# Performance work log

Hardware: AMD Instinct MI355X
Metric: run time of the kernel (lower is better)

Reference implementation:

```python
import jax, jax.numpy as jnp
import numpy as np

EPS = 1e-5
K = 3

def _bn(x, g, b):
    # training-mode BatchNorm2d: batch stats over (N,H,W), biased variance
    m = jnp.mean(x, axis=(0, 2, 3), keepdims=True)
    v = jnp.var(x, axis=(0, 2, 3), keepdims=True)
    return (x - m) * jax.lax.rsqrt(v + EPS) * g[None, :, None, None] + b[None, :, None, None]

def _gelu(x):
    return jax.nn.gelu(x, approximate=False)

def _dyn_dw(x, aw1, ab1, aw2, ab2):
    # dynamic depthwise conv: per-sample k^2 softmax weights shared over channels
    b, c, h, w = x.shape
    gap = jnp.mean(x, axis=(2, 3))                              # (b,c)
    h1 = jax.nn.relu(jnp.einsum('oc,bc->bo', aw1, gap) + ab1)   # (b,c//8)
    kw = jax.nn.softmax(jnp.einsum('oc,bc->bo', aw2, h1) + ab2, axis=1)  # (b,k^2)
    xp = jnp.pad(x, ((0, 0), (0, 0), (1, 1), (1, 1)))
    out = jnp.zeros_like(x)
    idx = 0
    for i in range(K):
        for j in range(K):
            out = out + kw[:, idx, None, None, None] * xp[:, :, i:i + h, j:j + w]
            idx += 1
    return out

def _channel_att(x, w1, w2):
    avg = jnp.mean(x, axis=(2, 3))        # (b,C)
    mx = jnp.max(x, axis=(2, 3))          # (b,C)
    def fc(v):
        return jnp.einsum('oc,bc->bo', w2, jax.nn.relu(jnp.einsum('oc,bc->bo', w1, v)))
    s = jax.nn.sigmoid(fc(avg) + fc(mx))  # (b,C)
    return s[:, :, None, None] * x

def _forward(x, w1, b1, g1, be1, aw1, ab1, aw2, ab2, g2, be2,
             ca_w1, ca_w2, pw, pb, g3, be3, sw, sb):
    b, n, d = x.shape
    h = w = int(np.sqrt(n))
    residual = x
    xi = jnp.transpose(x.reshape(b, h, w, d), (0, 3, 1, 2))       # (b,d,h,w)
    # pw_expand: 1x1 conv -> GELU -> BN
    y = jnp.einsum('oc,bchw->bohw', w1, xi) + b1[None, :, None, None]
    y = _bn(_gelu(y), g1, be1)                                    # (b,4d,h,w)
    # dw_conv: dynamic depthwise -> GELU -> BN -> channel attention
    y = _dyn_dw(y, aw1, ab1, aw2, ab2)
    y = _bn(_gelu(y), g2, be2)
    y = _channel_att(y, ca_w1, ca_w2)
    # spatial attention
    avg_o = jnp.mean(y, axis=1, keepdims=True)
    max_o = jnp.max(y, axis=1, keepdims=True)
    sp_in = jnp.concatenate([avg_o, max_o], axis=1)               # (b,2,h,w)
    sp = jax.lax.conv_general_dilated(sp_in, sw, (1, 1), ((3, 3), (3, 3)),
                                      dimension_numbers=('NCHW', 'OIHW', 'NCHW'))
    sp = jax.nn.sigmoid(sp + sb[None, :, None, None])
    y = y * sp
    # pw_project: 1x1 conv -> BN
    y = jnp.einsum('oc,bchw->bohw', pw, y) + pb[None, :, None, None]
    y = _bn(y, g3, be3)
    y = jnp.transpose(y, (0, 2, 3, 1)).reshape(b, n, d)
    return residual + y

def setup_inputs() -> dict:
    key = jax.random.key(0)
    ks = jax.random.split(key, 16)
    d, C = 256, 1024
    def rn(k, shape, fan):
        return jax.random.normal(k, shape, jnp.float32) * np.float32(np.sqrt(2.0 / fan))
    return {
        'x': jax.random.normal(ks[0], (8, 1024, d), jnp.float32),
        'w1': rn(ks[1], (C, d), d), 'b1': jnp.zeros((C,), jnp.float32),
        'g1': jnp.ones((C,), jnp.float32), 'be1': jnp.zeros((C,), jnp.float32),
        'aw1': rn(ks[2], (C // 8, C), C), 'ab1': jnp.zeros((C // 8,), jnp.float32),
        'aw2': rn(ks[3], (K * K, C // 8), C // 8), 'ab2': jnp.zeros((K * K,), jnp.float32),
        'g2': jnp.ones((C,), jnp.float32), 'be2': jnp.zeros((C,), jnp.float32),
        'ca_w1': rn(ks[4], (C // 16, C), C), 'ca_w2': rn(ks[5], (C, C // 16), C // 16),
        'pw': rn(ks[6], (d, C), C), 'pb': jnp.zeros((d,), jnp.float32),
        'g3': jnp.ones((d,), jnp.float32), 'be3': jnp.zeros((d,), jnp.float32),
        'sw': rn(ks[7], (1, 2, 7, 7), 2 * 49), 'sb': jnp.zeros((1,), jnp.float32),
    }

def reference(x, w1, b1, g1, be1, aw1, ab1, aw2, ab2, g2, be2,
              ca_w1, ca_w2, pw, pb, g3, be3, sw, sb):
    return _forward(x, w1, b1, g1, be1, aw1, ab1, aw2, ab2, g2, be2,
                    ca_w1, ca_w2, pw, pb, g3, be3, sw, sb)
```

## Files before the change

### kernel.cpp

```cpp
#include <hip/hip_runtime.h>
#include <math.h>

constexpr int B = 8;
constexpr int D = 256;
constexpr int C = 1024;
constexpr int H = 32, W = 32;
constexpr int P = H * W;
constexpr int M = B * P;
constexpr float EPS = 1e-5f;

typedef unsigned short u16;
typedef unsigned int u32;
typedef __attribute__((ext_vector_type(8))) short short8;
typedef __attribute__((ext_vector_type(4))) float floatx4;

constexpr size_t WS_CHSUM1 = 0;
constexpr size_t WS_CHSQ1  = 1024;
constexpr size_t WS_GAPSUM = 2048;
constexpr size_t WS_CHSUM3 = 10240;
constexpr size_t WS_CHSQ3  = 10496;
constexpr size_t WS_CHSUM2 = 10752;
constexpr size_t WS_CHSQ2  = 11776;
constexpr size_t WS_BSUM2  = 12800;
constexpr size_t WS_UMAX2  = 20992;
constexpr size_t WS_UMAXN2 = 29184;
constexpr size_t WS_ACC_COUNT = 37376;
constexpr size_t WS_SCALE1 = 37376;
constexpr size_t WS_SHIFT1 = 38400;
constexpr size_t WS_KW     = 39424;
constexpr size_t WS_SCALE2 = 39680;
constexpr size_t WS_SHIFT2 = 40704;
constexpr size_t WS_SATT   = 41728;
constexpr size_t WS_AVGO   = 49920;
constexpr size_t WS_MAXO   = 58112;
constexpr size_t WS_SP     = 66304;
constexpr size_t WS_PRE    = 74496;
constexpr size_t WS_T1B    = 2171648;
constexpr size_t WS_T2B    = 6365952;
constexpr size_t WS_XB     = 10560256;
constexpr size_t WS_W1B    = 11608832;
constexpr size_t WS_PWB    = 11739904;
constexpr size_t WS_PWBF   = 11870976;
constexpr size_t WS_BIAS2  = 12919552;

__device__ __forceinline__ float gelu_exact(float v) {
    return 0.5f * v * (1.0f + erff(v * 0.70710678118654752440f));
}

__device__ __forceinline__ u16 f2bf(float f) {
    u32 u = __float_as_uint(f);
    u += 0x7fff + ((u >> 16) & 1);
    return (u16)(u >> 16);
}

__device__ __forceinline__ float bf2f(u16 v) {
    return __uint_as_float(((u32)v) << 16);
}

__device__ __forceinline__ u32 fkey(float f) {
    u32 u = __float_as_uint(f);
    return (u & 0x80000000u) ? ~u : (u | 0x80000000u);
}
__device__ __forceinline__ float fkeyinv(u32 k) {
    return __uint_as_float((k & 0x80000000u) ? (k ^ 0x80000000u) : ~k);
}

#define GLOAD(SRC, DST) __builtin_amdgcn_global_load_lds( \
    (const __attribute__((address_space(1))) void*)(SRC), \
    (__attribute__((address_space(3))) void*)(DST), 16, 0, 0)

__global__ __launch_bounds__(256) void cvt_all_kernel(const float* __restrict__ x,
                                                      const float* __restrict__ w1,
                                                      u16* __restrict__ xb,
                                                      u16* __restrict__ w1b,
                                                      float* __restrict__ acc_zero) {
    const int i = blockIdx.x * 256 + threadIdx.x;
    if (i < (int)WS_ACC_COUNT) acc_zero[i] = 0.f;
    const float* src;
    u16* dst;
    int off;
    if (i < 524288) { src = x;  dst = xb;  off = i; }
    else            { src = w1; dst = w1b; off = i - 524288; }
    const float4 v = *(const float4*)(src + (size_t)off * 4);
    uint2 o;
    o.x = ((u32)f2bf(v.x)) | ((u32)f2bf(v.y) << 16);
    o.y = ((u32)f2bf(v.z)) | ((u32)f2bf(v.w) << 16);
    *(uint2*)(dst + (size_t)off * 4) = o;
}

template<int KD, int EPI, int NS, int MB, int NB>
__global__ __launch_bounds__(256) void mfma_gemm_kernel(
    const u16* __restrict__ A,
    const u16* __restrict__ Bw,
    const float* __restrict__ bias,
    const float* __restrict__ rowscale,
    void* __restrict__ outv,
    float* __restrict__ csum,
    float* __restrict__ csq,
    float* __restrict__ gsum)
{
    constexpr int MI = MB / 32;
    constexpr int NJ = NB / 32;
    constexpr int ABUF = MB * 32;
    constexpr int BBUF = NB * 32;
    constexpr int BUFSZ = ABUF + BBUF;
    constexpr int GA = MB / 64;
    constexpr int GB = NB / 64;
    constexpr int LD = GA + GB;
    constexpr int NCH = KD / 32;
    constexpr int GX = NS / NB;
    constexpr int NWG = (M / MB) * GX;
    constexpr int CPX = NWG / 8;
    extern __shared__ u16 smem[];
    const int t = threadIdx.x;
    const int lane = t & 63;

    const int lin = blockIdx.y * GX + blockIdx.x;
    const int swz = (lin & 7) * CPX + (lin >> 3);
    const int bx = swz % GX;
    const int by = swz / GX;
    const int row0 = by * MB;
    const int col0 = bx * NB;
    const int bb = row0 >> 10;

    const int wv = t >> 6;
    const int wrow = (wv >> 1) * (MB / 2);
    const int wcol = (wv & 1) * (NB / 2);
    const int lm = lane & 15;
    const int lk8 = (lane >> 4) * 8;
    const int srow = t >> 2;
    const int scol = (t & 3) * 8;
    const u16* gA = A + (size_t)(row0 + srow) * KD + scol;
    const u16* gB = Bw + (EPI == 1 ? (size_t)bb * NS * KD : (size_t)0)
                       + (size_t)(col0 + srow) * KD + scol;
    const float* biasp = bias + (EPI == 1 ? bb * NS : 0);

    const floatx4 zero = {0.f, 0.f, 0.f, 0.f};
    floatx4 acc[MI][NJ];
#pragma unroll
    for (int i = 0; i < MI; ++i)
#pragma unroll
        for (int j = 0; j < NJ; ++j) acc[i][j] = zero;

    auto stage = [&](u16* buf, int c) {
        const int kk = c * 32;
        u16* As = buf;
        u16* Bs = buf + ABUF;
#pragma unroll
        for (int g = 0; g < GA; ++g)
            GLOAD(gA + (size_t)g * 64 * KD + kk, As + g * 2048 + t * 8);
#pragma unroll
        for (int g = 0; g < GB; ++g)
            GLOAD(gB + (size_t)g * 64 * KD + kk, Bs + g * 2048 + t * 8);
    };
    auto compute = [&](const u16* buf) {
        const u16* As = buf;
        const u16* Bs = buf + ABUF;
        short8 af[MI], bf[NJ];
#pragma unroll
        for (int i = 0; i < MI; ++i)
            af[i] = *(const short8*)(As + (wrow + i * 16 + lm) * 32 + lk8);
#pragma unroll
        for (int j = 0; j < NJ; ++j)
            bf[j] = *(const short8*)(Bs + (wcol + j * 16 + lm) * 32 + lk8);
#pragma unroll
        for (int i = 0; i < MI; ++i)
#pragma unroll
            for (int j = 0; j < NJ; ++j)
                acc[i][j] = __builtin_amdgcn_mfma_f32_16x16x32_bf16(af[i], bf[j], acc[i][j], 0, 0, 0);
    };

    stage(smem, 0);
    for (int c = 0; c < NCH; ++c) {
        u16* curb = smem + (c & 1) * BUFSZ;
        if (c + 1 < NCH) {
            stage(smem + ((c + 1) & 1) * BUFSZ, c + 1);
            if constexpr (LD == 2) asm volatile("s_waitcnt vmcnt(2)" ::: "memory");
            else                   asm volatile("s_waitcnt vmcnt(3)" ::: "memory");
        } else {
            asm volatile("s_waitcnt vmcnt(0)" ::: "memory");
        }
        __builtin_amdgcn_s_barrier();
        compute(curb);
        asm volatile("s_waitcnt lgkmcnt(0)" ::: "memory");
        __builtin_amdgcn_s_barrier();
    }

    float colsum[NJ], colsq[NJ];
#pragma unroll
    for (int j = 0; j < NJ; ++j) { colsum[j] = 0.f; colsq[j] = 0.f; }

    if (EPI == 0) {
        u16* Cs = smem;
#pragma unroll
        for (int i = 0; i < MI; ++i) {
#pragma unroll
            for (int r = 0; r < 4; ++r) {
                const int lrow = wrow + i * 16 + (lane >> 4) * 4 + r;
#pragma unroll
                for (int j = 0; j < NJ; ++j) {
                    const int lcol = wcol + j * 16 + lm;
                    const float tv = gelu_exact(acc[i][j][r] + biasp[col0 + lcol]);
                    Cs[lrow * NB + lcol] = f2bf(tv);
                    colsum[j] += tv;
                    colsq[j] = fmaf(tv, tv, colsq[j]);
                }
            }
        }
        __syncthreads();
        constexpr int TPR = NB / 8;
        constexpr int RPP = 256 / TPR;
        u16* outp = (u16*)outv;
#pragma unroll
        for (int pp = 0; pp < MB / RPP; ++pp) {
            const int r = pp * RPP + t / TPR;
            const int cc = (t % TPR) * 8;
            *(uint4*)(outp + (size_t)(row0 + r) * NS + col0 + cc) =
                *(const uint4*)(Cs + r * NB + cc);
        }
    } else {
        float* Cs = (float*)smem;
#pragma unroll
        for (int i = 0; i < MI; ++i) {
#pragma unroll
            for (int r = 0; r < 4; ++r) {
                const int lrow = wrow + i * 16 + (lane >> 4) * 4 + r;
                const float rs = rowscale[row0 + lrow];
#pragma unroll
                for (int j = 0; j < NJ; ++j) {
                    const int lcol = wcol + j * 16 + lm;
                    const float tv = rs * (acc[i][j][r] + biasp[col0 + lcol]);
                    Cs[lrow * NB + lcol] = tv;
                    colsum[j] += tv;
                    colsq[j] = fmaf(tv, tv, colsq[j]);
                }
            }
        }
        __syncthreads();
        constexpr int TPR = NB / 4;
        constexpr int RPP = 256 / TPR;
        float* outp = (float*)outv;
#pragma unroll
        for (int pp = 0; pp < MB / RPP; ++pp) {
            const int r = pp * RPP + t / TPR;
            const int cc = (t % TPR) * 4;
            *(float4*)(outp + (size_t)(row0 + r) * NS + col0 + cc) =
                *(const float4*)(Cs + r * NB + cc);
        }
    }

#pragma unroll
    for (int j = 0; j < NJ; ++j) {
        float s = colsum[j];
        float q = colsq[j];
        s += __shfl_xor(s, 16); s += __shfl_xor(s, 32);
        q += __shfl_xor(q, 16); q += __shfl_xor(q, 32);
        if (lane < 16) {
            const int c = col0 + wcol + j * 16 + lm;
            atomicAdd(&csum[c], s);
            atomicAdd(&csq[c], q);
            if (EPI == 0) atomicAdd(&gsum[bb * NS + c], s);
        }
    }
}

__global__ __launch_bounds__(1024) void dynmlp_kernel(const float* __restrict__ chsum1,
                                                      const float* __restrict__ chsq1,
                                                      const float* __restrict__ gapsum,
                                                      const float* __restrict__ g1,
                                                      const float* __restrict__ be1,
                                                      const float* __restrict__ aw1,
                                                      const float* __restrict__ ab1,
                                                      const float* __restrict__ aw2,
                                                      const float* __restrict__ ab2,
                                                      float* __restrict__ scale1,
                                                      float* __restrict__ shift1,
                                                      float* __restrict__ kw) {
    const int b = blockIdx.x;
    const int t = threadIdx.x;
    const int wave = t >> 6, lane = t & 63;
    __shared__ float g[1024];
    __shared__ float h1[128];
    __shared__ float logits[12];
    {
        const float m = chsum1[t] * (1.0f / (float)M);
        const float var = chsq1[t] * (1.0f / (float)M) - m * m;
        const float rstd = rsqrtf(var + EPS);
        const float sc = rstd * g1[t];
        const float sh = be1[t] - m * sc;
        if (b == 0) { scale1[t] = sc; shift1[t] = sh; }
        g[t] = gapsum[b * C + t] * (1.0f / (float)P) * sc + sh;
    }
    __syncthreads();
#pragma unroll
    for (int k = 0; k < 8; ++k) {
        const int u = wave * 8 + k;
        const float4* wr = (const float4*)(aw1 + (size_t)u * C);
        float s = 0.f;
#pragma unroll
        for (int ch = 0; ch < 4; ++ch) {
            const float4 wv = wr[lane + 64 * ch];
            const float4 sv = *(const float4*)(g + 4 * lane + 256 * ch);
            s += wv.x * sv.x + wv.y * sv.y + wv.z * sv.z + wv.w * sv.w;
        }
#pragma unroll
        for (int off = 1; off < 64; off <<= 1) s += __shfl_xor(s, off);
        if (lane == 0) h1[u] = fmaxf(s + ab1[u], 0.f);
    }
    __syncthreads();
    if (wave < 9) {
        float s = aw2[wave * 128 + lane] * h1[lane]
                + aw2[wave * 128 + 64 + lane] * h1[64 + lane];
#pragma unroll
        for (int off = 1; off < 64; off <<= 1) s += __shfl_xor(s, off);
        if (lane == 0) logits[wave] = s + ab2[wave];
    }
    __syncthreads();
    if (t == 0) {
        float mx = logits[0];
        for (int i = 1; i < 9; ++i) mx = fmaxf(mx, logits[i]);
        float e[9], den = 0.f;
        for (int i = 0; i < 9; ++i) { e[i] = expf(logits[i] - mx); den += e[i]; }
        const float inv = 1.0f / den;
        for (int i = 0; i < 9; ++i) kw[b * 9 + i] = e[i] * inv;
    }
}

__global__ __launch_bounds__(256) void dwconv_kernel(const u16* __restrict__ t1b,
                                                     const float* __restrict__ scale1,
                                                     const float* __restrict__ shift1,
                                                     const float* __restrict__ kw,
                                                     u16* __restrict__ t2b,
                                                     float* __restrict__ chsum2,
                                                     float* __restrict__ chsq2,
                                                     float* __restrict__ bsum2,
                                                     u32* __restrict__ umax2,
                                                     u32* __restrict__ umaxn2) {
    __shared__ u16 rows[3 * 32 * 256];
    const int lin = blockIdx.y * 4 + blockIdx.x;
    const int swz = (lin & 7) * 128 + (lin >> 3);
    const int cq = swz & 3;
    const int bh = swz >> 2;
    const int b = bh >> 5;
    const int h = bh & 31;
    const int t = threadIdx.x;

    const u16* gbase = t1b + (size_t)b * P * C + cq * 256;
#pragma unroll
    for (int i = 0; i < 12; ++i) {
        const int lin2 = i * 256 + t;
        const int chunk = lin2 >> 5;
        const int r = chunk >> 5;
        const int w = chunk & 31;
        const int off8 = (lin2 & 31) * 8;
        const int hr = h + r - 1;
        uint4 v = {0u, 0u, 0u, 0u};
        if (hr >= 0 && hr < H)
            v = *(const uint4*)(gbase + (size_t)(hr * W + w) * C + off8);
        *(uint4*)(&rows[chunk * 256 + off8]) = v;
    }
    __syncthreads();

    const int c = t;
    const int gc = cq * 256 + c;
    float kk[9];
#pragma unroll
    for (int i = 0; i < 9; ++i) kk[i] = kw[b * 9 + i];
    const float sc = scale1[gc];
    const float sh = shift1[gc];
    float scm[3], shm[3];
    scm[0] = (h > 0)     ? sc : 0.f;  shm[0] = (h > 0)     ? sh : 0.f;
    scm[1] = sc;                      shm[1] = sh;
    scm[2] = (h < H - 1) ? sc : 0.f;  shm[2] = (h < H - 1) ? sh : 0.f;

    const u16* rp0 = rows + c;
#define DWVAL(ri, w) fmaf(bf2f(rp0[((ri) * 32 + (w)) * 256]), scm[ri], shm[ri])

    float vm0 = 0.f, vm1 = 0.f, vm2 = 0.f;
    float vc0 = DWVAL(0, 0), vc1 = DWVAL(1, 0), vc2 = DWVAL(2, 0);
    float vp0 = DWVAL(0, 1), vp1 = DWVAL(1, 1), vp2 = DWVAL(2, 1);

    float s = 0.f, q = 0.f, mx = -INFINITY, mn = INFINITY;
    u16* orow = t2b + ((size_t)b * P + h * W) * C + gc;
    for (int w = 0; w < W; ++w) {
        float acc;
        acc = kk[0] * vm0;
        acc = fmaf(kk[1], vc0, acc);
        acc = fmaf(kk[2], vp0, acc);
        acc = fmaf(kk[3], vm1, acc);
        acc = fmaf(kk[4], vc1, acc);
        acc = fmaf(kk[5], vp1, acc);
        acc = fmaf(kk[6], vm2, acc);
        acc = fmaf(kk[7], vc2, acc);
        acc = fmaf(kk[8], vp2, acc);
        const float y = gelu_exact(acc);
        orow[(size_t)w * C] = f2bf(y);
        s += y;
        q = fmaf(y, y, q);
        mx = fmaxf(mx, y);
        mn = fminf(mn, y);
        vm0 = vc0; vc0 = vp0;
        vm1 = vc1; vc1 = vp1;
        vm2 = vc2; vc2 = vp2;
        if (w + 2 < W) {
            vp0 = DWVAL(0, w + 2);
            vp1 = DWVAL(1, w + 2);
            vp2 = DWVAL(2, w + 2);
        } else {
            vp0 = 0.f; vp1 = 0.f; vp2 = 0.f;
        }
    }
#undef DWVAL
    atomicAdd(&chsum2[gc], s);
    atomicAdd(&chsq2[gc], q);
    atomicAdd(&bsum2[b * C + gc], s);
    atomicMax(&umax2[b * C + gc], fkey(mx));
    atomicMax(&umaxn2[b * C + gc], fkey(-mn));
}

__global__ __launch_bounds__(1024) void chatt_kernel(const float* __restrict__ chsum2,
                                                     const float* __restrict__ chsq2,
                                                     const float* __restrict__ bsum2,
                                                     const u32* __restrict__ umax2,
                                                     const u32* __restrict__ umaxn2,
                                                     const float* __restrict__ g2,
                                                     const float* __restrict__ be2,
                                                     const float* __restrict__ caw1,
                                                     const float* __restrict__ caw2,
                                                     float* __restrict__ scale2,
                                                     float* __restrict__ shift2,
                                                     float* __restrict__ s_att) {
    const int b = blockIdx.x;
    const int t = threadIdx.x;
    const int wave = t >> 6, lane = t & 63;
    __shared__ float la[1024], lx[1024], ha[64], hm[64];
    {
        const float m = chsum2[t] * (1.0f / (float)M);
        const float var = chsq2[t] * (1.0f / (float)M) - m * m;
        const float rstd = rsqrtf(var + EPS);
        const float sc = rstd * g2[t];
        const float sh = be2[t] - m * sc;
        if (b == 0) { scale2[t] = sc; shift2[t] = sh; }
        la[t] = bsum2[b * C + t] * (1.0f / (float)P) * sc + sh;
        const float mx = fkeyinv(umax2[b * C + t]);
        const float mn = -fkeyinv(umaxn2[b * C + t]);
        lx[t] = (sc >= 0.f ? mx : mn) * sc + sh;
    }
    __syncthreads();
#pragma unroll
    for (int k = 0; k < 8; ++k) {
        const int u = wave * 8 + k;
        const int row = u & 63;
        const float* src = (u < 64) ? la : lx;
        const float4* wr = (const float4*)(caw1 + (size_t)row * C);
        float s = 0.f;
#pragma unroll
        for (int ch = 0; ch < 4; ++ch) {
            const float4 wv = wr[lane + 64 * ch];
            const float4 sv = *(const float4*)(src + 4 * lane + 256 * ch);
            s += wv.x * sv.x + wv.y * sv.y + wv.z * sv.z + wv.w * sv.w;
        }
#pragma unroll
        for (int off = 1; off < 64; off <<= 1) s += __shfl_xor(s, off);
        if (lane == 0) {
            s = fmaxf(s, 0.f);
            if (u < 64) ha[row] = s; else hm[row] = s;
        }
    }
    __syncthreads();
    {
        const float4* w2 = (const float4*)(caw2 + (size_t)t * 64);
        float s = 0.f;
#pragma unroll
        for (int j = 0; j < 16; ++j) {
            const float4 wv = w2[j];
            s += wv.x * (ha[j * 4 + 0] + hm[j * 4 + 0]);
            s += wv.y * (ha[j * 4 + 1] + hm[j * 4 + 1]);
            s += wv.z * (ha[j * 4 + 2] + hm[j * 4 + 2]);
            s += wv.w * (ha[j * 4 + 3] + hm[j * 4 + 3]);
        }
        s_att[b * C + t] = 1.0f / (1.0f + expf(-s));
    }
}

__global__ __launch_bounds__(256) void fold_kernel(const float* __restrict__ pw,
                                                   const float* __restrict__ pb,
                                                   const float* __restrict__ scale2,
                                                   const float* __restrict__ shift2,
                                                   const float* __restrict__ s_att,
                                                   u16* __restrict__ pwb,
                                                   float* __restrict__ bias2) {
    const int bd = blockIdx.x;
    const int b = bd >> 8;
    const int d = bd & 255;
    const int t = threadIdx.x;
    const int c0 = t * 4;
    const float4 wv = *(const float4*)(pw + (size_t)d * C + c0);
    const float4 sc = *(const float4*)(scale2 + c0);
    const float4 sh = *(const float4*)(shift2 + c0);
    const float4 sa = *(const float4*)(s_att + (size_t)b * C + c0);
    uint2 o;
    o.x = ((u32)f2bf(wv.x * sc.x * sa.x)) | ((u32)f2bf(wv.y * sc.y * sa.y) << 16);
    o.y = ((u32)f2bf(wv.z * sc.z * sa.z)) | ((u32)f2bf(wv.w * sc.w * sa.w) << 16);
    *(uint2*)(pwb + ((size_t)b * D + d) * C + c0) = o;
    float s = wv.x * sh.x * sa.x + wv.y * sh.y * sa.y
            + wv.z * sh.z * sa.z + wv.w * sh.w * sa.w;
#pragma unroll
    for (int off = 1; off < 64; off <<= 1) s += __shfl_xor(s, off);
    __shared__ float ps[4];
    const int wave = t >> 6, lane = t & 63;
    if (lane == 0) ps[wave] = s;
    __syncthreads();
    if (t == 0) bias2[bd] = pb[d] + ps[0] + ps[1] + ps[2] + ps[3];
}

__global__ __launch_bounds__(256) void yq_kernel(const u16* __restrict__ t2b,
                                                 const float* __restrict__ scale2,
                                                 const float* __restrict__ shift2,
                                                 const float* __restrict__ s_att,
                                                 float* __restrict__ avg_o,
                                                 float* __restrict__ max_o) {
    const int row = blockIdx.x;
    const int b = row >> 10;
    const int t = threadIdx.x;
    const int c0 = t * 4;
    const uint2 vv = *(const uint2*)(t2b + (size_t)row * C + c0);
    const float v0 = bf2f((u16)(vv.x & 0xffff));
    const float v1 = bf2f((u16)(vv.x >> 16));
    const float v2 = bf2f((u16)(vv.y & 0xffff));
    const float v3 = bf2f((u16)(vv.y >> 16));
    const float4 sc = *(const float4*)(scale2 + c0);
    const float4 sh = *(const float4*)(shift2 + c0);
    const float4 sa = *(const float4*)(s_att + (size_t)b * C + c0);
    const float y0 = fmaf(v0, sc.x, sh.x) * sa.x;
    const float y1 = fmaf(v1, sc.y, sh.y) * sa.y;
    const float y2 = fmaf(v2, sc.z, sh.z) * sa.z;
    const float y3 = fmaf(v3, sc.w, sh.w) * sa.w;
    float s = (y0 + y1) + (y2 + y3);
    float mx = fmaxf(fmaxf(y0, y1), fmaxf(y2, y3));
#pragma unroll
    for (int off = 32; off > 0; off >>= 1) {
        s += __shfl_down(s, off);
        mx = fmaxf(mx, __shfl_down(mx, off));
    }
    __shared__ float ss[4], sm[4];
    const int wave = t >> 6, lane = t & 63;
    if (lane == 0) { ss[wave] = s; sm[wave] = mx; }
    __syncthreads();
    if (t == 0) {
        const float S = ss[0] + ss[1] + ss[2] + ss[3];
        const float Mx = fmaxf(fmaxf(sm[0], sm[1]), fmaxf(sm[2], sm[3]));
        avg_o[row] = S * (1.0f / (float)C);
        max_o[row] = Mx;
    }
}

__global__ __launch_bounds__(1024) void spconv_kernel(const float* __restrict__ avg_o,
                                                      const float* __restrict__ max_o,
                                                      const float* __restrict__ sw,
                                                      const float* __restrict__ sb,
                                                      float* __restrict__ sp) {
    const int b = blockIdx.x;
    const int t = threadIdx.x;
    __shared__ float pa[P], pm[P], wsh[98];
    pa[t] = avg_o[b * P + t];
    pm[t] = max_o[b * P + t];
    if (t < 98) wsh[t] = sw[t];
    const float sbv = sb[0];
    __syncthreads();
    const int h = t >> 5, w = t & 31;
    float acc = sbv;
#pragma unroll
    for (int i = 0; i < 7; ++i) {
        const int hh = h + i - 3;
        if (hh < 0 || hh >= H) continue;
#pragma unroll
        for (int j = 0; j < 7; ++j) {
            const int ww = w + j - 3;
            if (ww < 0 || ww >= W) continue;
            const int pidx = hh * W + ww;
            acc = fmaf(wsh[i * 7 + j], pa[pidx], acc);
            acc = fmaf(wsh[49 + i * 7 + j], pm[pidx], acc);
        }
    }
    sp[b * P + t] = 1.0f / (1.0f + expf(-acc));
}

__global__ __launch_bounds__(256) void final_kernel(const float* __restrict__ x,
                                                    const float* __restrict__ pre,
                                                    const float* __restrict__ chsum3,
                                                    const float* __restrict__ chsq3,
                                                    const float* __restrict__ g3,
                                                    const float* __restrict__ be3,
                                                    float* __restrict__ out) {
    __shared__ float lsc[256], lsh[256];
    const int t = threadIdx.x;
    {
        const float m = chsum3[t] * (1.0f / (float)M);
        const float var = chsq3[t] * (1.0f / (float)M) - m * m;
        const float rstd = rsqrtf(var + EPS);
        const float sc = rstd * g3[t];
        lsc[t] = sc;
        lsh[t] = be3[t] - m * sc;
    }
    __syncthreads();
    const int i = blockIdx.x * 256 + t;
    const int e = i * 4;
    const int d = e & 255;
    const float4 xv = *(const float4*)(x + e);
    const float4 pv = *(const float4*)(pre + e);
    const float4 sc = *(const float4*)(lsc + d);
    const float4 sh = *(const float4*)(lsh + d);
    float4 o;
    o.x = xv.x + fmaf(pv.x, sc.x, sh.x);
    o.y = xv.y + fmaf(pv.y, sc.y, sh.y);
    o.z = xv.z + fmaf(pv.z, sc.z, sh.z);
    o.w = xv.w + fmaf(pv.w, sc.w, sh.w);
    *(float4*)(out + e) = o;
}

extern "C" void kernel_launch(void* const* d_in, const int* in_sizes, int n_in,
                              void* d_out, int out_size, void* d_ws, size_t ws_size,
                              hipStream_t stream) {
    const float* x    = (const float*)d_in[0];
    const float* w1   = (const float*)d_in[1];
    const float* b1   = (const float*)d_in[2];
    const float* g1   = (const float*)d_in[3];
    const float* be1  = (const float*)d_in[4];
    const float* aw1  = (const float*)d_in[5];
    const float* ab1  = (const float*)d_in[6];
    const float* aw2  = (const float*)d_in[7];
    const float* ab2  = (const float*)d_in[8];
    const float* g2   = (const float*)d_in[9];
    const float* be2  = (const float*)d_in[10];
    const float* caw1 = (const float*)d_in[11];
    const float* caw2 = (const float*)d_in[12];
    const float* pw   = (const float*)d_in[13];
    const float* pb   = (const float*)d_in[14];
    const float* g3   = (const float*)d_in[15];
    const float* be3  = (const float*)d_in[16];
    const float* sw   = (const float*)d_in[17];
    const float* sb   = (const float*)d_in[18];
    float* out = (float*)d_out;
    float* ws = (float*)d_ws;

    float* chsum1  = ws + WS_CHSUM1;
    float* chsq1   = ws + WS_CHSQ1;
    float* gapsum  = ws + WS_GAPSUM;
    float* chsum3  = ws + WS_CHSUM3;
    float* chsq3   = ws + WS_CHSQ3;
    float* chsum2  = ws + WS_CHSUM2;
    float* chsq2   = ws + WS_CHSQ2;
    float* bsum2   = ws + WS_BSUM2;
    u32*   umax2   = (u32*)(ws + WS_UMAX2);
    u32*   umaxn2  = (u32*)(ws + WS_UMAXN2);
    float* scale1  = ws + WS_SCALE1;
    float* shift1  = ws + WS_SHIFT1;
    float* kw      = ws + WS_KW;
    float* scale2  = ws + WS_SCALE2;
    float* shift2  = ws + WS_SHIFT2;
    float* s_att   = ws + WS_SATT;
    float* avg_o   = ws + WS_AVGO;
    float* max_o   = ws + WS_MAXO;
    float* sp      = ws + WS_SP;
    float* pre     = ws + WS_PRE;
    float* bias2   = ws + WS_BIAS2;
    u16* t1b  = (u16*)(ws + WS_T1B);
    u16* t2b  = (u16*)(ws + WS_T2B);
    u16* xb   = (u16*)(ws + WS_XB);
    u16* w1b  = (u16*)(ws + WS_W1B);
    u16* pwbf = (u16*)(ws + WS_PWBF);

    cvt_all_kernel<<<dim3(2304), 256, 0, stream>>>(x, w1, xb, w1b, ws);
    mfma_gemm_kernel<256, 0, C, 128, 64><<<dim3(C / 64, M / 128), 256, 24576, stream>>>(
        xb, w1b, b1, nullptr, t1b, chsum1, chsq1, gapsum);
    dynmlp_kernel<<<dim3(B), 1024, 0, stream>>>(chsum1, chsq1, gapsum, g1, be1,
                                                aw1, ab1, aw2, ab2, scale1, shift1, kw);
    dwconv_kernel<<<dim3(4, B * H), 256, 0, stream>>>(t1b, scale1, shift1, kw, t2b,
                                                      chsum2, chsq2, bsum2, umax2, umaxn2);
    chatt_kernel<<<dim3(B), 1024, 0, stream>>>(chsum2, chsq2, bsum2, umax2, umaxn2,
                                               g2, be2, caw1, caw2, scale2, shift2, s_att);
    fold_kernel<<<dim3(B * D), 256, 0, stream>>>(pw, pb, scale2, shift2, s_att, pwbf, bias2);
    yq_kernel<<<dim3(M), 256, 0, stream>>>(t2b, scale2, shift2, s_att, avg_o, max_o);
    spconv_kernel<<<dim3(B), 1024, 0, stream>>>(avg_o, max_o, sw, sb, sp);
    mfma_gemm_kernel<1024, 1, D, 128, 64><<<dim3(D / 64, M / 128), 256, 32768, stream>>>(
        t2b, pwbf, bias2, sp, pre, chsum3, chsq3, nullptr);
    final_kernel<<<dim3((M * D / 4) / 256), 256, 0, stream>>>(x, pre, chsum3, chsq3, g3, be3, out);
}
```

Measured before the change: 205.3 us.

## Fuse spatial conv into projection GEMM prologue and merge yq/fold kernels

The 7x7 spatial-attention conv and sigmoid are now computed inside the second GEMM, using a small halo of avg/max rows staged in extra shared memory. The pb bias is moved out of the fold into a post-scale bias in the epilogue. The yq and fold kernels are merged into a single launch with a combined grid. Together these remove two kernel launches and the sp round trip through global memory, at the cost of extra shared memory and a redundant per-block conv prologue.

```diff
diff --git a/kernel.cpp b/kernel.cpp
--- a/kernel.cpp
+++ b/kernel.cpp
@@ -93,7 +93,11 @@
     const u16* __restrict__ A,
     const u16* __restrict__ Bw,
     const float* __restrict__ bias,
-    const float* __restrict__ rowscale,
+    const float* __restrict__ bias_post,
+    const float* __restrict__ avg_o,
+    const float* __restrict__ max_o,
+    const float* __restrict__ swp,
+    const float* __restrict__ sbp,
     void* __restrict__ outv,
     float* __restrict__ csum,
     float* __restrict__ csq,
@@ -171,6 +175,41 @@
     };
 
     stage(smem, 0);
+
+    float* ext = (float*)smem + 8192;
+    if constexpr (EPI == 1) {
+        const int p0 = (by & 7) * MB;
+        const int h0 = p0 >> 5;
+        const int bbase = bb * P;
+        for (int e = t; e < 640; e += 256) {
+            const bool isM = e >= 320;
+            const int idx = isM ? e - 320 : e;
+            const int r = idx >> 5, w = idx & 31;
+            const int hh = h0 - 3 + r;
+            float v = 0.f;
+            if (hh >= 0 && hh < H) v = (isM ? max_o : avg_o)[bbase + hh * W + w];
+            ext[e] = v;
+        }
+        if (t < 98) ext[640 + t] = swp[t];
+        __syncthreads();
+        if (t < 128) {
+            const int hl = t >> 5, w = t & 31;
+            float a = sbp[0];
+#pragma unroll
+            for (int i = 0; i < 7; ++i) {
+                const int r = hl + i;
+#pragma unroll
+                for (int j = 0; j < 7; ++j) {
+                    const int ww = w + j - 3;
+                    if (ww < 0 || ww >= W) continue;
+                    a = fmaf(ext[640 + i * 7 + j], ext[r * 32 + ww], a);
+                    a = fmaf(ext[640 + 49 + i * 7 + j], ext[320 + r * 32 + ww], a);
+                }
+            }
+            ext[768 + t] = 1.0f / (1.0f + expf(-a));
+        }
+    }
+
     for (int c = 0; c < NCH; ++c) {
         u16* curb = smem + (c & 1) * BUFSZ;
         if (c + 1 < NCH) {
@@ -225,11 +264,12 @@
 #pragma unroll
             for (int r = 0; r < 4; ++r) {
                 const int lrow = wrow + i * 16 + (lane >> 4) * 4 + r;
-                const float rs = rowscale[row0 + lrow];
+                const float rs = ext[768 + lrow];
 #pragma unroll
                 for (int j = 0; j < NJ; ++j) {
                     const int lcol = wcol + j * 16 + lm;
-                    const float tv = rs * (acc[i][j][r] + biasp[col0 + lcol]);
+                    const float tv = rs * (acc[i][j][r] + biasp[col0 + lcol])
+                                   + bias_post[col0 + lcol];
                     Cs[lrow * NB + lcol] = tv;
                     colsum[j] += tv;
                     colsq[j] = fmaf(tv, tv, colsq[j]);
@@ -483,107 +523,71 @@
     }
 }
 
-__global__ __launch_bounds__(256) void fold_kernel(const float* __restrict__ pw,
-                                                   const float* __restrict__ pb,
-                                                   const float* __restrict__ scale2,
-                                                   const float* __restrict__ shift2,
-                                                   const float* __restrict__ s_att,
-                                                   u16* __restrict__ pwb,
-                                                   float* __restrict__ bias2) {
-    const int bd = blockIdx.x;
-    const int b = bd >> 8;
-    const int d = bd & 255;
+__global__ __launch_bounds__(256) void yqfold_kernel(const u16* __restrict__ t2b,
+                                                     const float* __restrict__ scale2,
+                                                     const float* __restrict__ shift2,
+                                                     const float* __restrict__ s_att,
+                                                     const float* __restrict__ pw,
+                                                     float* __restrict__ avg_o,
+                                                     float* __restrict__ max_o,
+                                                     u16* __restrict__ pwb,
+                                                     float* __restrict__ bias2) {
+    const int bid = blockIdx.x;
     const int t = threadIdx.x;
-    const int c0 = t * 4;
-    const float4 wv = *(const float4*)(pw + (size_t)d * C + c0);
-    const float4 sc = *(const float4*)(scale2 + c0);
-    const float4 sh = *(const float4*)(shift2 + c0);
-    const float4 sa = *(const float4*)(s_att + (size_t)b * C + c0);
-    uint2 o;
-    o.x = ((u32)f2bf(wv.x * sc.x * sa.x)) | ((u32)f2bf(wv.y * sc.y * sa.y) << 16);
-    o.y = ((u32)f2bf(wv.z * sc.z * sa.z)) | ((u32)f2bf(wv.w * sc.w * sa.w) << 16);
-    *(uint2*)(pwb + ((size_t)b * D + d) * C + c0) = o;
-    float s = wv.x * sh.x * sa.x + wv.y * sh.y * sa.y
-            + wv.z * sh.z * sa.z + wv.w * sh.w * sa.w;
-#pragma unroll
-    for (int off = 1; off < 64; off <<= 1) s += __shfl_xor(s, off);
-    __shared__ float ps[4];
     const int wave = t >> 6, lane = t & 63;
-    if (lane == 0) ps[wave] = s;
-    __syncthreads();
-    if (t == 0) bias2[bd] = pb[d] + ps[0] + ps[1] + ps[2] + ps[3];
-}
-
-__global__ __launch_bounds__(256) void yq_kernel(const u16* __restrict__ t2b,
-                                                 const float* __restrict__ scale2,
-                                                 const float* __restrict__ shift2,
-                                                 const float* __restrict__ s_att,
-                                                 float* __restrict__ avg_o,
-                                                 float* __restrict__ max_o) {
-    const int row = blockIdx.x;
-    const int b = row >> 10;
-    const int t = threadIdx.x;
-    const int c0 = t * 4;
-    const uint2 vv = *(const uint2*)(t2b + (size_t)row * C + c0);
-    const float v0 = bf2f((u16)(vv.x & 0xffff));
-    const float v1 = bf2f((u16)(vv.x >> 16));
-    const float v2 = bf2f((u16)(vv.y & 0xffff));
-    const float v3 = bf2f((u16)(vv.y >> 16));
-    const float4 sc = *(const float4*)(scale2 + c0);
-    const float4 sh = *(const float4*)(shift2 + c0);
-    const float4 sa = *(const float4*)(s_att + (size_t)b * C + c0);
-    const float y0 = fmaf(v0, sc.x, sh.x) * sa.x;
-    const float y1 = fmaf(v1, sc.y, sh.y) * sa.y;
-    const float y2 = fmaf(v2, sc.z, sh.z) * sa.z;
-    const float y3 = fmaf(v3, sc.w, sh.w) * sa.w;
-    float s = (y0 + y1) + (y2 + y3);
-    float mx = fmaxf(fmaxf(y0, y1), fmaxf(y2, y3));
-#pragma unroll
-    for (int off = 32; off > 0; off >>= 1) {
-        s += __shfl_down(s, off);
-        mx = fmaxf(mx, __shfl_down(mx, off));
-    }
-    __shared__ float ss[4], sm[4];
-    const int wave = t >> 6, lane = t & 63;
-    if (lane == 0) { ss[wave] = s; sm[wave] = mx; }
-    __syncthreads();
-    if (t == 0) {
-        const float S = ss[0] + ss[1] + ss[2] + ss[3];
-        const float Mx = fmaxf(fmaxf(sm[0], sm[1]), fmaxf(sm[2], sm[3]));
-        avg_o[row] = S * (1.0f / (float)C);
-        max_o[row] = Mx;
-    }
-}
-
-__global__ __launch_bounds__(1024) void spconv_kernel(const float* __restrict__ avg_o,
-                                                      const float* __restrict__ max_o,
-                                                      const float* __restrict__ sw,
-                                                      const float* __restrict__ sb,
-                                                      float* __restrict__ sp) {
-    const int b = blockIdx.x;
-    const int t = threadIdx.x;
-    __shared__ float pa[P], pm[P], wsh[98];
-    pa[t] = avg_o[b * P + t];
-    pm[t] = max_o[b * P + t];
-    if (t < 98) wsh[t] = sw[t];
-    const float sbv = sb[0];
-    __syncthreads();
-    const int h = t >> 5, w = t & 31;
-    float acc = sbv;
-#pragma unroll
-    for (int i = 0; i < 7; ++i) {
-        const int hh = h + i - 3;
-        if (hh < 0 || hh >= H) continue;
-#pragma unroll
-        for (int j = 0; j < 7; ++j) {
-            const int ww = w + j - 3;
-            if (ww < 0 || ww >= W) continue;
-            const int pidx = hh * W + ww;
-            acc = fmaf(wsh[i * 7 + j], pa[pidx], acc);
-            acc = fmaf(wsh[49 + i * 7 + j], pm[pidx], acc);
-        }
-    }
-    sp[b * P + t] = 1.0f / (1.0f + expf(-acc));
+    __shared__ float r0[4], r1[4];
+    if (bid < M) {
+        const int row = bid;
+        const int b = row >> 10;
+        const int c0 = t * 4;
+        const uint2 vv = *(const uint2*)(t2b + (size_t)row * C + c0);
+        const float v0 = bf2f((u16)(vv.x & 0xffff));
+        const float v1 = bf2f((u16)(vv.x >> 16));
+        const float v2 = bf2f((u16)(vv.y & 0xffff));
+        const float v3 = bf2f((u16)(vv.y >> 16));
+        const float4 sc = *(const float4*)(scale2 + c0);
+        const float4 sh = *(const float4*)(shift2 + c0);
+        const float4 sa = *(const float4*)(s_att + (size_t)b * C + c0);
+        const float y0 = fmaf(v0, sc.x, sh.x) * sa.x;
+        const float y1 = fmaf(v1, sc.y, sh.y) * sa.y;
+        const float y2 = fmaf(v2, sc.z, sh.z) * sa.z;
+        const float y3 = fmaf(v3, sc.w, sh.w) * sa.w;
+        float s = (y0 + y1) + (y2 + y3);
+        float mx = fmaxf(fmaxf(y0, y1), fmaxf(y2, y3));
+#pragma unroll
+        for (int off = 32; off > 0; off >>= 1) {
+            s += __shfl_down(s, off);
+            mx = fmaxf(mx, __shfl_down(mx, off));
+        }
+        if (lane == 0) { r0[wave] = s; r1[wave] = mx; }
+        __syncthreads();
+        if (t == 0) {
+            const float S = r0[0] + r0[1] + r0[2] + r0[3];
+            const float Mx = fmaxf(fmaxf(r1[0], r1[1]), fmaxf(r1[2], r1[3]));
+            avg_o[row] = S * (1.0f / (float)C);
+            max_o[row] = Mx;
+        }
+    } else {
+        const int bd = bid - M;
+        const int b = bd >> 8;
+        const int d = bd & 255;
+        const int c0 = t * 4;
+        const float4 wv = *(const float4*)(pw + (size_t)d * C + c0);
+        const float4 sc = *(const float4*)(scale2 + c0);
+        const float4 sh = *(const float4*)(shift2 + c0);
+        const float4 sa = *(const float4*)(s_att + (size_t)b * C + c0);
+        uint2 o;
+        o.x = ((u32)f2bf(wv.x * sc.x * sa.x)) | ((u32)f2bf(wv.y * sc.y * sa.y) << 16);
+        o.y = ((u32)f2bf(wv.z * sc.z * sa.z)) | ((u32)f2bf(wv.w * sc.w * sa.w) << 16);
+        *(uint2*)(pwb + ((size_t)b * D + d) * C + c0) = o;
+        float s = wv.x * sh.x * sa.x + wv.y * sh.y * sa.y
+                + wv.z * sh.z * sa.z + wv.w * sh.w * sa.w;
+#pragma unroll
+        for (int off = 1; off < 64; off <<= 1) s += __shfl_xor(s, off);
+        if (lane == 0) r0[wave] = s;
+        __syncthreads();
+        if (t == 0) bias2[bd] = r0[0] + r0[1] + r0[2] + r0[3];
+    }
 }
 
 __global__ __launch_bounds__(256) void final_kernel(const float* __restrict__ x,
@@ -662,7 +666,6 @@
     float* s_att   = ws + WS_SATT;
     float* avg_o   = ws + WS_AVGO;
     float* max_o   = ws + WS_MAXO;
-    float* sp      = ws + WS_SP;
     float* pre     = ws + WS_PRE;
     float* bias2   = ws + WS_BIAS2;
     u16* t1b  = (u16*)(ws + WS_T1B);
@@ -673,17 +676,18 @@
 
     cvt_all_kernel<<<dim3(2304), 256, 0, stream>>>(x, w1, xb, w1b, ws);
     mfma_gemm_kernel<256, 0, C, 128, 64><<<dim3(C / 64, M / 128), 256, 24576, stream>>>(
-        xb, w1b, b1, nullptr, t1b, chsum1, chsq1, gapsum);
+        xb, w1b, b1, nullptr, nullptr, nullptr, nullptr, nullptr,
+        t1b, chsum1, chsq1, gapsum);
     dynmlp_kernel<<<dim3(B), 1024, 0, stream>>>(chsum1, chsq1, gapsum, g1, be1,
                                                 aw1, ab1, aw2, ab2, scale1, shift1, kw);
     dwconv_kernel<<<dim3(4, B * H), 256, 0, stream>>>(t1b, scale1, shift1, kw, t2b,
                                                       chsum2, chsq2, bsum2, umax2, umaxn2);
     chatt_kernel<<<dim3(B), 1024, 0, stream>>>(chsum2, chsq2, bsum2, umax2, umaxn2,
                                                g2, be2, caw1, caw2, scale2, shift2, s_att);
-    fold_kernel<<<dim3(B * D), 256, 0, stream>>>(pw, pb, scale2, shift2, s_att, pwbf, bias2);
-    yq_kernel<<<dim3(M), 256, 0, stream>>>(t2b, scale2, shift2, s_att, avg_o, max_o);
-    spconv_kernel<<<dim3(B), 1024, 0, stream>>>(avg_o, max_o, sw, sb, sp);
-    mfma_gemm_kernel<1024, 1, D, 128, 64><<<dim3(D / 64, M / 128), 256, 32768, stream>>>(
-        t2b, pwbf, bias2, sp, pre, chsum3, chsq3, nullptr);
+    yqfold_kernel<<<dim3(M + B * D), 256, 0, stream>>>(t2b, scale2, shift2, s_att, pw,
+                                                       avg_o, max_o, pwbf, bias2);
+    mfma_gemm_kernel<1024, 1, D, 128, 64><<<dim3(D / 64, M / 128), 256, 36352, stream>>>(
+        t2b, pwbf, bias2, pb, avg_o, max_o, sw, sb,
+        pre, chsum3, chsq3, nullptr);
     final_kernel<<<dim3((M * D / 4) / 256), 256, 0, stream>>>(x, pre, chsum3, chsq3, g3, be3, out);
 }
```

After: 202.2 us. Within noise of the previous version (-1.5%).
